# Kernel tuning notes

Measured on AMD Instinct MI355X. Metric: run time of the kernel, lower is better.

The kernel has to match this reference:

```python
import jax, jax.numpy as jnp
import numpy as np

B, C, Z, H, W = 16, 1, 1, 512, 512
N_ITER = 128
STEP = 0.97 / 3.0  # 0.97 / stacked_operator_norm, used for both primal and dual stepsizes
DIMS = (-2, -1)


def _fft2c(x):
    # MRpro FastFourierOp convention: centered orthonormal FFT
    return jnp.fft.fftshift(jnp.fft.fftn(jnp.fft.ifftshift(x, DIMS), axes=DIMS, norm='ortho'), DIMS)


def _ifft2c(k):
    return jnp.fft.fftshift(jnp.fft.ifftn(jnp.fft.ifftshift(k, DIMS), axes=DIMS, norm='ortho'), DIMS)


def _fgrad(x):
    # forward finite differences with circular padding, stacked along a new leading dim
    return jnp.stack([jnp.roll(x, -1, axis=d) - x for d in DIMS], axis=0)


def _fgrad_adj(p):
    # adjoint of forward circular difference: backward difference (negative divergence)
    return sum(jnp.roll(p[i], 1, axis=d) - p[i] for i, d in enumerate(DIMS))


def setup_inputs() -> dict:
    key = jax.random.key(0)
    k1, k2, k3, k4, k5, k6 = jax.random.split(key, 6)
    shape = (B, C, Z, H, W)
    initial_image_r = jax.random.normal(k1, shape, jnp.float32)
    initial_image_i = jax.random.normal(k2, shape, jnp.float32)
    kdata_r = jax.random.normal(k3, shape, jnp.float32)
    kdata_i = jax.random.normal(k4, shape, jnp.float32)
    mask = jax.random.randint(k5, (1, 1, 1, H, W), 0, 2).astype(jnp.int32)
    # strictly positive spatially adaptive regularization parameter map
    lam = jax.random.uniform(k6, shape, jnp.float32, minval=1e-3, maxval=0.1)
    return {'initial_image_r': initial_image_r, 'initial_image_i': initial_image_i,
            'kdata_r': kdata_r, 'kdata_i': kdata_i, 'lam': lam, 'mask': mask}


def reference(initial_image_r, initial_image_i, kdata_r, kdata_i, lam, mask):
    x = jax.lax.complex(initial_image_r, initial_image_i)
    y = jax.lax.complex(kdata_r, kdata_i)
    m = mask.astype(jnp.float32)
    sigma = jnp.float32(STEP)
    tau = jnp.float32(STEP)

    p1 = jnp.zeros_like(y)                      # dual for data term (k-space shape)
    p2 = jnp.zeros((2,) + x.shape, x.dtype)     # dual for TV term (2 gradient components)
    xbar = x

    def body(carry, _):
        x, xbar, p1, p2 = carry
        # dual ascent + prox of conjugates
        p1 = p1 + sigma * (m * _fft2c(xbar))
        p1 = (p1 - sigma * y) / (1.0 + sigma)          # prox_{sigma f1*}, f1 = 0.5||.-y||^2
        q = p2 + sigma * _fgrad(xbar)
        # prox_{sigma f2*}, f2 = ||lam .||_1 viewed as real: clamp real & imag to [-lam, lam]
        p2 = jax.lax.complex(jnp.clip(q.real, -lam, lam), jnp.clip(q.imag, -lam, lam))
        # primal descent (g = 0 so prox is identity) + extrapolation (theta = 1)
        x_new = x - tau * (_ifft2c(m * p1) + _fgrad_adj(p2))
        xbar = 2.0 * x_new - x
        return (x_new, xbar, p1, p2), None

    (x, xbar, p1, p2), _ = jax.lax.scan(body, (x, xbar, p1, p2), None, length=N_ITER)
    # return complex solution as stacked (real, imag) float tensor
    return jnp.stack((x.real, x.imag), axis=-1)
```

## Files before the change

### kernel.cpp

```cpp
#include <hip/hip_runtime.h>
#include <hip/hip_fp16.h>
#include <cstddef>

#define NBATCH 16
#define NSIDE  512
#define NT     (NBATCH * NSIDE * NSIDE)
#define NLINES 8
#define LSTRIDE 577
#define APACK  (512 * 512)

constexpr float SIGMA = (float)(0.97 / 3.0);
constexpr float TAU   = (float)(0.97 / 3.0);
constexpr float INV1S = (float)(1.0 / (1.0 + 0.97 / 3.0));
constexpr float INV_N = 1.0f / 512.0f;

__device__ __forceinline__ float2 cadd(float2 a, float2 b){ return make_float2(a.x+b.x, a.y+b.y); }
__device__ __forceinline__ float2 csub(float2 a, float2 b){ return make_float2(a.x-b.x, a.y-b.y); }
__device__ __forceinline__ float2 cmul(float2 a, float2 b){ return make_float2(a.x*b.x - a.y*b.y, a.x*b.y + a.y*b.x); }

__device__ __forceinline__ int SL(int s){ return s + (s >> 3); }
__device__ __forceinline__ int rev9(int s){ return ((s & 7) << 6) | (s & 56) | (s >> 6); }

__device__ __forceinline__ unsigned h2bits(float2 v){
  __half2 h = __floats2half2_rn(v.x, v.y);
  return *reinterpret_cast<unsigned*>(&h);
}
__device__ __forceinline__ float2 bits2f(unsigned u){
  __half2 h = *reinterpret_cast<__half2*>(&u);
  return __half22float2(h);
}

template<int S>
__device__ __forceinline__ void dft8(float2 v[8]){
  const float RS = 0.70710678118654752440f;
  float2 a0 = cadd(v[0], v[4]), a4 = csub(v[0], v[4]);
  float2 a1 = cadd(v[1], v[5]), a5 = csub(v[1], v[5]);
  float2 a2 = cadd(v[2], v[6]), a6 = csub(v[2], v[6]);
  float2 a3 = cadd(v[3], v[7]), a7 = csub(v[3], v[7]);
  a5 = cmul(a5, make_float2(RS, (float)S * RS));
  a6 = make_float2(-(float)S * a6.y, (float)S * a6.x);
  a7 = cmul(a7, make_float2(-RS, (float)S * RS));
  float2 b0 = cadd(a0, a2), b2 = csub(a0, a2);
  float2 b1 = cadd(a1, a3), b3 = csub(a1, a3);
  b3 = make_float2(-(float)S * b3.y, (float)S * b3.x);
  v[0] = cadd(b0, b1); v[4] = csub(b0, b1);
  v[2] = cadd(b2, b3); v[6] = csub(b2, b3);
  float2 c0 = cadd(a4, a6), c2 = csub(a4, a6);
  float2 c1 = cadd(a5, a7), c3 = csub(a5, a7);
  c3 = make_float2(-(float)S * c3.y, (float)S * c3.x);
  v[1] = cadd(c0, c1); v[5] = csub(c0, c1);
  v[3] = cadd(c2, c3); v[7] = csub(c2, c3);
}

__device__ __forceinline__ void fft_fwd_pair(float2* __restrict__ A, float2* __restrict__ B, int l){
  float2 va[8], vb[8];
  #pragma unroll
  for(int j = 0; j < 8; j++){ int s = SL(l + 64*j); va[j] = A[s]; vb[j] = B[s]; }
  dft8<-1>(va); dft8<-1>(vb);
  #pragma unroll
  for(int t = 1; t < 8; t++){
    float sn, cs;
    __sincosf((-6.283185307179586f / 512.0f) * (float)(l * t), &sn, &cs);
    float2 w = make_float2(cs, sn);
    va[t] = cmul(va[t], w); vb[t] = cmul(vb[t], w);
  }
  #pragma unroll
  for(int t = 0; t < 8; t++){ int s = SL(t*64 + l); A[s] = va[t]; B[s] = vb[t]; }
  __syncthreads();
  int tg = l >> 3, m = l & 7;
  #pragma unroll
  for(int j = 0; j < 8; j++){ int s = SL(tg*64 + m + 8*j); va[j] = A[s]; vb[j] = B[s]; }
  dft8<-1>(va); dft8<-1>(vb);
  #pragma unroll
  for(int t = 1; t < 8; t++){
    float sn, cs;
    __sincosf((-6.283185307179586f / 64.0f) * (float)(m * t), &sn, &cs);
    float2 w = make_float2(cs, sn);
    va[t] = cmul(va[t], w); vb[t] = cmul(vb[t], w);
  }
  #pragma unroll
  for(int t = 0; t < 8; t++){ int s = SL(tg*64 + t*8 + m); A[s] = va[t]; B[s] = vb[t]; }
  __syncthreads();
  #pragma unroll
  for(int j = 0; j < 8; j++){ int s = SL(8*l + j); va[j] = A[s]; vb[j] = B[s]; }
  dft8<-1>(va); dft8<-1>(vb);
  #pragma unroll
  for(int t = 0; t < 8; t++){ int s = SL(8*l + t); A[s] = va[t]; B[s] = vb[t]; }
}

__device__ __forceinline__ void fft_inv_pair(float2* __restrict__ A, float2* __restrict__ B, int l){
  float2 va[8], vb[8];
  #pragma unroll
  for(int j = 0; j < 8; j++){ int s = SL(8*l + j); va[j] = A[s]; vb[j] = B[s]; }
  dft8<1>(va); dft8<1>(vb);
  #pragma unroll
  for(int t = 0; t < 8; t++){ int s = SL(8*l + t); A[s] = va[t]; B[s] = vb[t]; }
  __syncthreads();
  int tg = l >> 3, m = l & 7;
  #pragma unroll
  for(int j = 0; j < 8; j++){ int s = SL(tg*64 + 8*j + m); va[j] = A[s]; vb[j] = B[s]; }
  #pragma unroll
  for(int j = 1; j < 8; j++){
    float sn, cs;
    __sincosf((6.283185307179586f / 64.0f) * (float)(m * j), &sn, &cs);
    float2 w = make_float2(cs, sn);
    va[j] = cmul(va[j], w); vb[j] = cmul(vb[j], w);
  }
  dft8<1>(va); dft8<1>(vb);
  #pragma unroll
  for(int j = 0; j < 8; j++){ int s = SL(tg*64 + m + 8*j); A[s] = va[j]; B[s] = vb[j]; }
  __syncthreads();
  #pragma unroll
  for(int t = 0; t < 8; t++){ int s = SL(t*64 + l); va[t] = A[s]; vb[t] = B[s]; }
  #pragma unroll
  for(int t = 1; t < 8; t++){
    float sn, cs;
    __sincosf((6.283185307179586f / 512.0f) * (float)(l * t), &sn, &cs);
    float2 w = make_float2(cs, sn);
    va[t] = cmul(va[t], w); vb[t] = cmul(vb[t], w);
  }
  dft8<1>(va); dft8<1>(vb);
  #pragma unroll
  for(int j = 0; j < 8; j++){ int s = SL(l + 64*j); A[s] = va[j]; B[s] = vb[j]; }
}

__device__ __forceinline__ void store_strip_h(const float2* __restrict__ lds, __half2* __restrict__ dst, int t){
  int q = t & 3, s0v = t >> 2;
  #pragma unroll
  for(int k = 0; k < 8; k++){
    int s = s0v + 64 * k;
    float2 v0 = lds[(2*q)   * LSTRIDE + SL(s)];
    float2 v1 = lds[(2*q+1) * LSTRIDE + SL(s)];
    uint2 u; u.x = h2bits(v0); u.y = h2bits(v1);
    *reinterpret_cast<uint2*>(dst + ((size_t)s << 9) + 2*q) = u;
  }
}

__device__ __forceinline__ void load_strip_h(float2* __restrict__ lds, const __half2* __restrict__ src, int t){
  int rr = t >> 5, col = t & 31;
  #pragma unroll
  for(int k = 0; k < 8; k++){
    int e = 2*col + 64*k;
    uint2 u = *reinterpret_cast<const uint2*>(src + ((size_t)rr << 9) + e);
    lds[rr * LSTRIDE + SL(e)]     = bits2f(u.x);
    lds[rr * LSTRIDE + SL(e + 1)] = bits2f(u.y);
  }
}

__global__ __launch_bounds__(256) void k_fwd_rows(const float2* __restrict__ xbar, __half2* __restrict__ U){
  __shared__ float2 lds[NLINES * LSTRIDE];
  int b = blockIdx.x >> 6, r0 = (blockIdx.x & 63) << 3;
  int t = threadIdx.x;
  int rr = t >> 5, col = t & 31;
  const float2* src = xbar + ((size_t)(b * 512 + r0) << 9);
  #pragma unroll
  for(int k = 0; k < 16; k++){
    int c = col + 32 * k;
    float2 v = src[(rr << 9) + c];
    float sc = ((r0 + rr + c) & 1) ? -INV_N : INV_N;
    v.x *= sc; v.y *= sc;
    lds[rr * LSTRIDE + SL(c)] = v;
  }
  __syncthreads();
  int wv = t >> 6, l = t & 63;
  fft_fwd_pair(&lds[wv * LSTRIDE], &lds[(wv + 4) * LSTRIDE], l);
  __syncthreads();
  store_strip_h(lds, U + ((size_t)b << 18) + r0, t);
}

__global__ __launch_bounds__(256) void k_colsA(const __half2* __restrict__ U, __half2* __restrict__ p1p,
                                               const __half2* __restrict__ yp, const int* __restrict__ idx,
                                               const int* __restrict__ cnt, __half2* __restrict__ V,
                                               const float2* __restrict__ xbar, __half2* __restrict__ p2h,
                                               __half2* __restrict__ p2w, const __half* __restrict__ lamh){
  __shared__ float2 lds[NLINES * LSTRIDE];
  int b = blockIdx.x >> 6, cs0 = (blockIdx.x & 63) << 3;
  int t = threadIdx.x;
  int rr = t >> 5, col = t & 31;
  load_strip_h(lds, U + ((size_t)(b * 512 + cs0) << 9), t);
  __syncthreads();
  int wv = t >> 6, l = t & 63;
  fft_fwd_pair(&lds[wv * LSTRIDE], &lds[(wv + 4) * LSTRIDE], l);
  __syncthreads();
  int g = rr, lane = col;
  int cs = cs0 + g;
  int jbase = cs << 9;
  int jcnt = cnt[cs];
  size_t boff = (size_t)b * APACK;
  int ksi[16]; float2 pn[16];
  #pragma unroll
  for(int tt = 0; tt < 16; tt++){
    int jj = lane + 32 * tt;
    bool act = jj < jcnt;
    int j = jbase + (act ? jj : 0);
    int ks = act ? idx[j] : 0;
    float2 K = lds[g * LSTRIDE + SL(ks)];
    float2 yv = __half22float2(yp[boff + j]);
    float2 p  = __half22float2(p1p[boff + j]);
    float2 v;
    v.x = (p.x + SIGMA * (K.x - yv.x)) * INV1S;
    v.y = (p.y + SIGMA * (K.y - yv.y)) * INV1S;
    if(act) p1p[boff + j] = __floats2half2_rn(v.x, v.y);
    ksi[tt] = act ? ks : -1;
    pn[tt] = v;
  }
  __syncthreads();
  #pragma unroll
  for(int k = 0; k < 16; k++) lds[rr * LSTRIDE + SL(col + 32 * k)] = make_float2(0.0f, 0.0f);
  __syncthreads();
  #pragma unroll
  for(int tt = 0; tt < 16; tt++) if(ksi[tt] >= 0) lds[g * LSTRIDE + SL(ksi[tt])] = pn[tt];
  __syncthreads();
  fft_inv_pair(&lds[wv * LSTRIDE], &lds[(wv + 4) * LSTRIDE], l);
  __syncthreads();
  store_strip_h(lds, V + ((size_t)b << 18) + cs0, t);

  int base_i = blockIdx.x << 12;
  #pragma unroll
  for(int k = 0; k < 16; k++){
    int i = base_i + (k << 8) + t;
    int c = i & 511, r = (i >> 9) & 511;
    int idn = (r < 511) ? i + 512 : i - (511 << 9);
    int irt = (c < 511) ? i + 1   : i - 511;
    float2 xc = xbar[i];
    float2 xd = xbar[idn];
    float2 xr = xbar[irt];
    float lv = __half2float(lamh[i]);
    float2 qh = __half22float2(p2h[i]);
    float2 qw = __half22float2(p2w[i]);
    qh.x += SIGMA * (xd.x - xc.x); qh.y += SIGMA * (xd.y - xc.y);
    qw.x += SIGMA * (xr.x - xc.x); qw.y += SIGMA * (xr.y - xc.y);
    qh.x = fminf(fmaxf(qh.x, -lv), lv); qh.y = fminf(fmaxf(qh.y, -lv), lv);
    qw.x = fminf(fmaxf(qw.x, -lv), lv); qw.y = fminf(fmaxf(qw.y, -lv), lv);
    p2h[i] = __floats2half2_rn(qh.x, qh.y);
    p2w[i] = __floats2half2_rn(qw.x, qw.y);
  }
}

__global__ __launch_bounds__(256) void k_megaB(const __half2* __restrict__ V, const __half2* __restrict__ p2h,
                                               const __half2* __restrict__ p2w, float2* __restrict__ x,
                                               float2* __restrict__ xbar, __half2* __restrict__ U, int last){
  __shared__ float2 lds[NLINES * LSTRIDE];
  int b = blockIdx.x >> 6, r0 = (blockIdx.x & 63) << 3;
  int t = threadIdx.x;
  int rr = t >> 5, col = t & 31;
  load_strip_h(lds, V + ((size_t)(b * 512 + r0) << 9), t);
  __syncthreads();
  int wv = t >> 6, l = t & 63;
  fft_inv_pair(&lds[wv * LSTRIDE], &lds[(wv + 4) * LSTRIDE], l);
  __syncthreads();
  int r = r0 + rr;
  size_t base   = ((size_t)(b * 512 + r) << 9);
  size_t baseUp = ((size_t)(b * 512 + ((r - 1) & 511)) << 9);
  #pragma unroll
  for(int k = 0; k < 16; k++){
    int c = col + 32 * k;
    int cl = (c - 1) & 511;
    float2 v = lds[rr * LSTRIDE + SL(c)];
    float sc = ((r + c) & 1) ? -INV_N : INV_N;
    float2 ph  = __half22float2(p2h[base + c]);
    float2 phu = __half22float2(p2h[baseUp + c]);
    float2 pw  = __half22float2(p2w[base + c]);
    float2 pwl = __half22float2(p2w[base + cl]);
    float gx = sc * v.x + (phu.x - ph.x) + (pwl.x - pw.x);
    float gy = sc * v.y + (phu.y - ph.y) + (pwl.y - pw.y);
    float2 xo = x[base + c];
    float2 xn = make_float2(xo.x - TAU * gx, xo.y - TAU * gy);
    x[base + c] = xn;
    float2 xb2 = make_float2(2.0f * xn.x - xo.x, 2.0f * xn.y - xo.y);
    xbar[base + c] = xb2;
    lds[rr * LSTRIDE + SL(c)] = make_float2(sc * xb2.x, sc * xb2.y);
  }
  if(last) return;
  __syncthreads();
  fft_fwd_pair(&lds[wv * LSTRIDE], &lds[(wv + 4) * LSTRIDE], l);
  __syncthreads();
  store_strip_h(lds, U + ((size_t)b << 18) + r0, t);
}

__global__ __launch_bounds__(256) void k_init_x(const float* __restrict__ ir, const float* __restrict__ ii,
                                                float2* __restrict__ x, float2* __restrict__ xbar){
  int i = blockIdx.x * 256 + threadIdx.x;
  float2 v = make_float2(ir[i], ii[i]);
  x[i] = v; xbar[i] = v;
}

__global__ __launch_bounds__(256) void k_init_lam(const float* __restrict__ lam, __half* __restrict__ lamh){
  int i = blockIdx.x * 256 + threadIdx.x;
  lamh[i] = __float2half(lam[i]);
}

__global__ __launch_bounds__(256) void k_pack(const int* __restrict__ mask, const float* __restrict__ kr,
                                              const float* __restrict__ ki, int* __restrict__ idx,
                                              int* __restrict__ cnt, __half2* __restrict__ yp){
  __shared__ int wcnt[8];
  int cs = blockIdx.x;
  int t = threadIdx.x, lane = t & 63, wv = t >> 6;
  int csr = rev9(cs);
  int jbase = cs << 9;
  #pragma unroll
  for(int rnd = 0; rnd < 2; rnd++){
    int ks = t + 256 * rnd;
    int ksr = rev9(ks);
    int pred = (mask[(ksr << 9) + csr] != 0) ? 1 : 0;
    unsigned long long bal = __ballot(pred);
    if(lane == 0) wcnt[4 * rnd + wv] = (int)__popcll(bal);
    __syncthreads();
    int pre = 0;
    for(int w = 0; w < wv; w++) pre += wcnt[4 * rnd + w];
    int roundbase = (rnd == 1) ? (wcnt[0] + wcnt[1] + wcnt[2] + wcnt[3]) : 0;
    int lpre = (int)__popcll(bal & ((1ull << lane) - 1ull));
    if(pred){
      int pos = jbase + roundbase + pre + lpre;
      idx[pos] = ks;
      float s = ((ksr + csr) & 1) ? -1.0f : 1.0f;
      for(int b = 0; b < 16; b++){
        size_t a = ((size_t)b << 18) + ((size_t)ksr << 9) + csr;
        yp[(size_t)b * APACK + pos] = __floats2half2_rn(s * kr[a], s * ki[a]);
      }
    }
    __syncthreads();
  }
  if(t == 0) cnt[cs] = wcnt[0] + wcnt[1] + wcnt[2] + wcnt[3] + wcnt[4] + wcnt[5] + wcnt[6] + wcnt[7];
}

extern "C" void kernel_launch(void* const* d_in, const int* in_sizes, int n_in,
                              void* d_out, int out_size, void* d_ws, size_t ws_size,
                              hipStream_t stream){
  const float* ir  = (const float*)d_in[0];
  const float* ii  = (const float*)d_in[1];
  const float* kdr = (const float*)d_in[2];
  const float* kdi = (const float*)d_in[3];
  const float* lam = (const float*)d_in[4];
  const int*  mask = (const int*)d_in[5];
  float2* x = (float2*)d_out;

  char* ws = (char*)d_ws;
  __half2* p1p  = (__half2*)ws;
  __half2* yp   = p1p + (size_t)APACK * 16;
  __half2* p2h  = yp  + (size_t)APACK * 16;
  __half2* p2w  = p2h + NT;
  __half2* U    = p2w + NT;
  __half2* V    = U   + NT;
  float2*  xbar = (float2*)(V + NT);
  __half*  lamh = (__half*)(xbar + NT);
  int*     idx  = (int*)(lamh + NT);
  int*     cnt  = idx + APACK;

  hipMemsetAsync(p1p, 0, (size_t)APACK * 16 * sizeof(__half2), stream);
  hipMemsetAsync(p2h, 0, (size_t)2 * NT * sizeof(__half2), stream);
  k_pack<<<512, 256, 0, stream>>>(mask, kdr, kdi, idx, cnt, yp);
  k_init_lam<<<NT / 256, 256, 0, stream>>>(lam, lamh);
  k_init_x<<<NT / 256, 256, 0, stream>>>(ir, ii, x, xbar);
  k_fwd_rows<<<1024, 256, 0, stream>>>(xbar, U);

  for(int it = 0; it < 128; it++){
    k_colsA<<<1024, 256, 0, stream>>>(U, p1p, yp, idx, cnt, V, xbar, p2h, p2w, lamh);
    k_megaB<<<1024, 256, 0, stream>>>(V, p2h, p2w, x, xbar, U, it == 127 ? 1 : 0);
  }
}
```

Before: 8.455 ms.

## Tile the intermediate FFT buffers into 8x8 blocks and store xbar in fp16

The intermediate U/V spectra move from a strided transposed row layout to a blocked layout of 8-line tiles. Row-strip stores and column-strip loads then become contiguous 16-byte accesses instead of scattered 8-byte ones. xbar is also kept only in half precision, which halves its traffic in both the write in megaB and the gradient reads in colsA. The first row FFT now reads the raw inputs directly. The cost is lower precision in the TV dual update, which feeds fp16 xbar into the gradient.

```diff
diff --git a/kernel.cpp b/kernel.cpp
--- a/kernel.cpp
+++ b/kernel.cpp
@@ -124,7 +124,7 @@
   for(int j = 0; j < 8; j++){ int s = SL(l + 64*j); A[s] = va[j]; B[s] = vb[j]; }
 }
 
-__device__ __forceinline__ void store_strip_h(const float2* __restrict__ lds, __half2* __restrict__ dst, int t){
+__device__ __forceinline__ void store_strip_blk(const float2* __restrict__ lds, __half2* __restrict__ tile, int t){
   int q = t & 3, s0v = t >> 2;
   #pragma unroll
   for(int k = 0; k < 8; k++){
@@ -132,52 +132,57 @@
     float2 v0 = lds[(2*q)   * LSTRIDE + SL(s)];
     float2 v1 = lds[(2*q+1) * LSTRIDE + SL(s)];
     uint2 u; u.x = h2bits(v0); u.y = h2bits(v1);
-    *reinterpret_cast<uint2*>(dst + ((size_t)s << 9) + 2*q) = u;
-  }
-}
-
-__device__ __forceinline__ void load_strip_h(float2* __restrict__ lds, const __half2* __restrict__ src, int t){
-  int rr = t >> 5, col = t & 31;
-  #pragma unroll
-  for(int k = 0; k < 8; k++){
-    int e = 2*col + 64*k;
-    uint2 u = *reinterpret_cast<const uint2*>(src + ((size_t)rr << 9) + e);
-    lds[rr * LSTRIDE + SL(e)]     = bits2f(u.x);
-    lds[rr * LSTRIDE + SL(e + 1)] = bits2f(u.y);
-  }
-}
-
-__global__ __launch_bounds__(256) void k_fwd_rows(const float2* __restrict__ xbar, __half2* __restrict__ U){
+    *reinterpret_cast<uint2*>(tile + s*8 + 2*q) = u;
+  }
+}
+
+__device__ __forceinline__ void load_strip_blk(float2* __restrict__ lds, const __half2* __restrict__ base,
+                                               int lineBase, int t){
+  #pragma unroll
+  for(int k = 0; k < 4; k++){
+    int idx = t + 256 * k;
+    int tb = idx >> 4;
+    int rem = idx & 15;
+    int g = rem >> 1, h = rem & 1;
+    uint4 u = *reinterpret_cast<const uint4*>(base + ((size_t)tb << 12) + ((lineBase + g) << 3) + (h << 2));
+    int n = (tb << 3) + (h << 2);
+    lds[g * LSTRIDE + SL(n)]     = bits2f(u.x);
+    lds[g * LSTRIDE + SL(n + 1)] = bits2f(u.y);
+    lds[g * LSTRIDE + SL(n + 2)] = bits2f(u.z);
+    lds[g * LSTRIDE + SL(n + 3)] = bits2f(u.w);
+  }
+}
+
+__global__ __launch_bounds__(256) void k_fwd_rows(const float* __restrict__ ir, const float* __restrict__ ii,
+                                                  __half2* __restrict__ U){
   __shared__ float2 lds[NLINES * LSTRIDE];
-  int b = blockIdx.x >> 6, r0 = (blockIdx.x & 63) << 3;
+  int b = blockIdx.x >> 6, rb = blockIdx.x & 63, r0 = rb << 3;
   int t = threadIdx.x;
   int rr = t >> 5, col = t & 31;
-  const float2* src = xbar + ((size_t)(b * 512 + r0) << 9);
+  size_t base = ((size_t)(b * 512 + r0 + rr) << 9);
   #pragma unroll
   for(int k = 0; k < 16; k++){
     int c = col + 32 * k;
-    float2 v = src[(rr << 9) + c];
     float sc = ((r0 + rr + c) & 1) ? -INV_N : INV_N;
-    v.x *= sc; v.y *= sc;
-    lds[rr * LSTRIDE + SL(c)] = v;
+    lds[rr * LSTRIDE + SL(c)] = make_float2(sc * ir[base + c], sc * ii[base + c]);
   }
   __syncthreads();
   int wv = t >> 6, l = t & 63;
   fft_fwd_pair(&lds[wv * LSTRIDE], &lds[(wv + 4) * LSTRIDE], l);
   __syncthreads();
-  store_strip_h(lds, U + ((size_t)b << 18) + r0, t);
+  store_strip_blk(lds, U + ((size_t)(b * 64 + rb) << 12), t);
 }
 
 __global__ __launch_bounds__(256) void k_colsA(const __half2* __restrict__ U, __half2* __restrict__ p1p,
                                                const __half2* __restrict__ yp, const int* __restrict__ idx,
                                                const int* __restrict__ cnt, __half2* __restrict__ V,
-                                               const float2* __restrict__ xbar, __half2* __restrict__ p2h,
+                                               const __half2* __restrict__ xbarh, __half2* __restrict__ p2h,
                                                __half2* __restrict__ p2w, const __half* __restrict__ lamh){
   __shared__ float2 lds[NLINES * LSTRIDE];
-  int b = blockIdx.x >> 6, cs0 = (blockIdx.x & 63) << 3;
+  int b = blockIdx.x >> 6, cb = blockIdx.x & 63, cs0 = cb << 3;
   int t = threadIdx.x;
   int rr = t >> 5, col = t & 31;
-  load_strip_h(lds, U + ((size_t)(b * 512 + cs0) << 9), t);
+  load_strip_blk(lds, U + ((size_t)b << 18), cs0, t);
   __syncthreads();
   int wv = t >> 6, l = t & 63;
   fft_fwd_pair(&lds[wv * LSTRIDE], &lds[(wv + 4) * LSTRIDE], l);
@@ -213,7 +218,7 @@
   __syncthreads();
   fft_inv_pair(&lds[wv * LSTRIDE], &lds[(wv + 4) * LSTRIDE], l);
   __syncthreads();
-  store_strip_h(lds, V + ((size_t)b << 18) + cs0, t);
+  store_strip_blk(lds, V + ((size_t)(b * 64 + cb) << 12), t);
 
   int base_i = blockIdx.x << 12;
   #pragma unroll
@@ -222,9 +227,9 @@
     int c = i & 511, r = (i >> 9) & 511;
     int idn = (r < 511) ? i + 512 : i - (511 << 9);
     int irt = (c < 511) ? i + 1   : i - 511;
-    float2 xc = xbar[i];
-    float2 xd = xbar[idn];
-    float2 xr = xbar[irt];
+    float2 xc = __half22float2(xbarh[i]);
+    float2 xd = __half22float2(xbarh[idn]);
+    float2 xr = __half22float2(xbarh[irt]);
     float lv = __half2float(lamh[i]);
     float2 qh = __half22float2(p2h[i]);
     float2 qw = __half22float2(p2w[i]);
@@ -239,12 +244,12 @@
 
 __global__ __launch_bounds__(256) void k_megaB(const __half2* __restrict__ V, const __half2* __restrict__ p2h,
                                                const __half2* __restrict__ p2w, float2* __restrict__ x,
-                                               float2* __restrict__ xbar, __half2* __restrict__ U, int last){
+                                               __half2* __restrict__ xbarh, __half2* __restrict__ U, int last){
   __shared__ float2 lds[NLINES * LSTRIDE];
-  int b = blockIdx.x >> 6, r0 = (blockIdx.x & 63) << 3;
+  int b = blockIdx.x >> 6, rb = blockIdx.x & 63, r0 = rb << 3;
   int t = threadIdx.x;
   int rr = t >> 5, col = t & 31;
-  load_strip_h(lds, V + ((size_t)(b * 512 + r0) << 9), t);
+  load_strip_blk(lds, V + ((size_t)b << 18), r0, t);
   __syncthreads();
   int wv = t >> 6, l = t & 63;
   fft_inv_pair(&lds[wv * LSTRIDE], &lds[(wv + 4) * LSTRIDE], l);
@@ -268,21 +273,22 @@
     float2 xn = make_float2(xo.x - TAU * gx, xo.y - TAU * gy);
     x[base + c] = xn;
     float2 xb2 = make_float2(2.0f * xn.x - xo.x, 2.0f * xn.y - xo.y);
-    xbar[base + c] = xb2;
+    xbarh[base + c] = __floats2half2_rn(xb2.x, xb2.y);
     lds[rr * LSTRIDE + SL(c)] = make_float2(sc * xb2.x, sc * xb2.y);
   }
   if(last) return;
   __syncthreads();
   fft_fwd_pair(&lds[wv * LSTRIDE], &lds[(wv + 4) * LSTRIDE], l);
   __syncthreads();
-  store_strip_h(lds, U + ((size_t)b << 18) + r0, t);
+  store_strip_blk(lds, U + ((size_t)(b * 64 + rb) << 12), t);
 }
 
 __global__ __launch_bounds__(256) void k_init_x(const float* __restrict__ ir, const float* __restrict__ ii,
-                                                float2* __restrict__ x, float2* __restrict__ xbar){
+                                                float2* __restrict__ x, __half2* __restrict__ xbarh){
   int i = blockIdx.x * 256 + threadIdx.x;
-  float2 v = make_float2(ir[i], ii[i]);
-  x[i] = v; xbar[i] = v;
+  float vr = ir[i], vi = ii[i];
+  x[i] = make_float2(vr, vi);
+  xbarh[i] = __floats2half2_rn(vr, vi);
 }
 
 __global__ __launch_bounds__(256) void k_init_lam(const float* __restrict__ lam, __half* __restrict__ lamh){
@@ -336,26 +342,26 @@
   float2* x = (float2*)d_out;
 
   char* ws = (char*)d_ws;
-  __half2* p1p  = (__half2*)ws;
-  __half2* yp   = p1p + (size_t)APACK * 16;
-  __half2* p2h  = yp  + (size_t)APACK * 16;
-  __half2* p2w  = p2h + NT;
-  __half2* U    = p2w + NT;
-  __half2* V    = U   + NT;
-  float2*  xbar = (float2*)(V + NT);
-  __half*  lamh = (__half*)(xbar + NT);
-  int*     idx  = (int*)(lamh + NT);
-  int*     cnt  = idx + APACK;
+  __half2* p1p   = (__half2*)ws;
+  __half2* yp    = p1p + (size_t)APACK * 16;
+  __half2* p2h   = yp  + (size_t)APACK * 16;
+  __half2* p2w   = p2h + NT;
+  __half2* U     = p2w + NT;
+  __half2* V     = U   + NT;
+  __half2* xbarh = V   + NT;
+  __half*  lamh  = (__half*)(xbarh + NT);
+  int*     idx   = (int*)(lamh + NT);
+  int*     cnt   = idx + APACK;
 
   hipMemsetAsync(p1p, 0, (size_t)APACK * 16 * sizeof(__half2), stream);
   hipMemsetAsync(p2h, 0, (size_t)2 * NT * sizeof(__half2), stream);
   k_pack<<<512, 256, 0, stream>>>(mask, kdr, kdi, idx, cnt, yp);
   k_init_lam<<<NT / 256, 256, 0, stream>>>(lam, lamh);
-  k_init_x<<<NT / 256, 256, 0, stream>>>(ir, ii, x, xbar);
-  k_fwd_rows<<<1024, 256, 0, stream>>>(xbar, U);
+  k_init_x<<<NT / 256, 256, 0, stream>>>(ir, ii, x, xbarh);
+  k_fwd_rows<<<1024, 256, 0, stream>>>(ir, ii, U);
 
   for(int it = 0; it < 128; it++){
-    k_colsA<<<1024, 256, 0, stream>>>(U, p1p, yp, idx, cnt, V, xbar, p2h, p2w, lamh);
-    k_megaB<<<1024, 256, 0, stream>>>(V, p2h, p2w, x, xbar, U, it == 127 ? 1 : 0);
-  }
-}
+    k_colsA<<<1024, 256, 0, stream>>>(U, p1p, yp, idx, cnt, V, xbarh, p2h, p2w, lamh);
+    k_megaB<<<1024, 256, 0, stream>>>(V, p2h, p2w, x, xbarh, U, it == 127 ? 1 : 0);
+  }
+}
```

Result: faster. 7.307 ms (-13.6%).
